# Optimization experiments

Measured on AMD Instinct MI355X. Metric: run time of the kernel, lower is better.

The kernel has to match this reference:

```python
import jax, jax.numpy as jnp
import numpy as np

EPS = 1e-5

def exp_map_zero(v):
    # Poincare ball exp map at origin: tanh(||v||) * v / ||v||
    norm = jnp.clip(jnp.linalg.norm(v, axis=-1, keepdims=True), EPS, None)
    return jnp.tanh(jnp.clip(norm, None, 15.0)) * v / norm

def poincare_pairwise_distance(x, c):
    # x: [N, D] points in the ball, c: [K, D] points in the ball -> [N, K]
    x2 = jnp.sum(x * x, axis=-1)                      # [N]
    c2 = jnp.sum(c * c, axis=-1)                      # [K]
    sqdiff = x2[:, None] + c2[None, :] - 2.0 * (x @ c.T)   # ||x-c||^2, [N, K]
    sqdiff = jnp.clip(sqdiff, 0.0, None)
    denom = jnp.clip((1.0 - x2)[:, None] * (1.0 - c2)[None, :], EPS, None)
    arg = jnp.clip(1.0 + 2.0 * sqdiff / denom, 1.0 + 1e-7, None)
    return jnp.arccosh(arg)

def setup_inputs() -> dict:
    key = jax.random.key(0)
    k1, k2, k3 = jax.random.split(key, 3)
    N, K, D = 200000, 128, 128
    node_repr = jax.random.normal(k1, (N, D), dtype=jnp.float32) * 0.05  # inside unit ball
    mask = jnp.ones((N, 1), dtype=jnp.float32)
    centroid_weight = jax.random.normal(k2, (K, D), dtype=jnp.float32) * 0.05
    return {"node_repr": node_repr, "mask": mask, "centroid_weight": centroid_weight}

def reference(node_repr, mask, centroid_weight):
    # euclidean embed_manifold path: map centroid params onto the ball first
    centroid_repr = exp_map_zero(centroid_weight)                  # [K, D]
    dist = poincare_pairwise_distance(node_repr, centroid_repr)    # [N, K]
    node_centroid_dist = dist[None, :, :] * mask                   # [1, N, K] (mask [N,1] broadcasts)
    graph_centroid_dist = jnp.sum(node_centroid_dist, axis=1) / jnp.sum(mask)  # [1, K]
    return (graph_centroid_dist, node_centroid_dist)
```

## Files before the change

### kernel.cpp

```cpp
#include <hip/hip_runtime.h>
#include <hip/hip_bf16.h>
#include <math.h>

#define EPSF 1e-5f

constexpr int D = 128;
constexpr int K = 128;
constexpr int ROWS_PER_BLOCK = 64;

typedef __bf16 bf16x8 __attribute__((ext_vector_type(8)));
typedef float  f32x4  __attribute__((ext_vector_type(4)));

__global__ __launch_bounds__(64) void prep_kernel(const float* __restrict__ w,
                                                  __bf16* __restrict__ crb,
                                                  float* __restrict__ c2) {
    int k = blockIdx.x;
    int t = threadIdx.x;
    float a = w[k * D + t];
    float b = w[k * D + t + 64];
    float ss = a * a + b * b;
#pragma unroll
    for (int off = 1; off < 64; off <<= 1)
        ss += __shfl_xor(ss, off, 64);
    float nrm   = sqrtf(ss);
    float nclip = fmaxf(nrm, EPSF);
    float targ  = fminf(nclip, 15.0f);
    float th    = tanhf(targ);
    float s     = th / nclip;
    crb[k * D + t]      = (__bf16)(a * s);
    crb[k * D + t + 64] = (__bf16)(b * s);
    if (t == 0) {
        float cn = s * nrm;
        c2[k] = cn * cn;
    }
}

__global__ __launch_bounds__(256) void main_kernel(
        const float* __restrict__ x, const float* __restrict__ mask,
        const __bf16* __restrict__ crb, const float* __restrict__ c2g,
        float* __restrict__ out_node, float* __restrict__ partial,
        float* __restrict__ maskpart, int N) {
    __shared__ float sX2[ROWS_PER_BLOCK];
    __shared__ float sMask[ROWS_PER_BLOCK];
    __shared__ float sC2[K];
    __shared__ float sCol[4][K];

    const int t    = threadIdx.x;
    const int wave = t >> 6;
    const int lane = t & 63;
    const int m    = lane & 15;
    const int q    = lane >> 4;
    const int nbase   = blockIdx.x * ROWS_PER_BLOCK;
    const int rowbase = nbase + wave * 16;

    if (t < ROWS_PER_BLOCK) sMask[t] = mask[nbase + t];
    if (t < K) sC2[t] = c2g[t];

    const float*  xrow = x + (size_t)(rowbase + m) * D + q * 8;
    const __bf16* cb   = crb + (size_t)m * D + q * 8;

    f32x4 acc[8] = {};
    float ssq = 0.f;

#pragma unroll
    for (int s = 0; s < 4; s++) {
        float4 a0 = *(const float4*)(xrow + s * 32);
        float4 a1 = *(const float4*)(xrow + s * 32 + 4);
        ssq += a0.x*a0.x + a0.y*a0.y + a0.z*a0.z + a0.w*a0.w
             + a1.x*a1.x + a1.y*a1.y + a1.z*a1.z + a1.w*a1.w;
        bf16x8 av;
        av[0] = (__bf16)a0.x; av[1] = (__bf16)a0.y;
        av[2] = (__bf16)a0.z; av[3] = (__bf16)a0.w;
        av[4] = (__bf16)a1.x; av[5] = (__bf16)a1.y;
        av[6] = (__bf16)a1.z; av[7] = (__bf16)a1.w;
#pragma unroll
        for (int tk = 0; tk < 8; tk++) {
            bf16x8 bv = *(const bf16x8*)(cb + ((size_t)tk * 16) * D + s * 32);
            acc[tk] = __builtin_amdgcn_mfma_f32_16x16x32_bf16(av, bv, acc[tk], 0, 0, 0);
        }
    }

    ssq += __shfl_xor(ssq, 16, 64);
    ssq += __shfl_xor(ssq, 32, 64);
    if (lane < 16) sX2[wave * 16 + lane] = ssq;
    __syncthreads();

    float x2r[4], pxr[4], mvr[4];
#pragma unroll
    for (int i = 0; i < 4; i++) {
        int rl = wave * 16 + q * 4 + i;
        x2r[i] = sX2[rl];
        pxr[i] = 1.0f - x2r[i];
        mvr[i] = sMask[rl];
    }

    float colsum[8] = {0.f, 0.f, 0.f, 0.f, 0.f, 0.f, 0.f, 0.f};
#pragma unroll
    for (int tk = 0; tk < 8; tk++) {
        int col = tk * 16 + m;
        float c2v = sC2[col];
        float pc  = 1.0f - c2v;
#pragma unroll
        for (int i = 0; i < 4; i++) {
            int n = rowbase + q * 4 + i;
            float dot = acc[tk][i];
            float sq  = fmaxf(x2r[i] + c2v - 2.0f * dot, 0.0f);
            float den = fmaxf(pxr[i] * pc, EPSF);
            float arg = fmaf(2.0f * sq, __builtin_amdgcn_rcpf(den), 1.0f);
            arg = fmaxf(arg, 1.0f + 1e-7f);
            float dist = __logf(arg + __builtin_amdgcn_sqrtf(fmaf(arg, arg, -1.0f)));
            float val = dist * mvr[i];
            out_node[(size_t)n * K + col] = val;
            colsum[tk] += val;
        }
    }

#pragma unroll
    for (int tk = 0; tk < 8; tk++) {
        colsum[tk] += __shfl_xor(colsum[tk], 16, 64);
        colsum[tk] += __shfl_xor(colsum[tk], 32, 64);
    }
    if (lane < 16) {
#pragma unroll
        for (int tk = 0; tk < 8; tk++)
            sCol[wave][tk * 16 + lane] = colsum[tk];
    }
    __syncthreads();
    if (t < K)
        partial[(size_t)blockIdx.x * K + t] =
            sCol[0][t] + sCol[1][t] + sCol[2][t] + sCol[3][t];
    if (t == 0) {
        float msum = 0.f;
#pragma unroll
        for (int r = 0; r < ROWS_PER_BLOCK; r++) msum += sMask[r];
        maskpart[blockIdx.x] = msum;
    }
}

__global__ __launch_bounds__(256) void reduce_kernel(
        const float* __restrict__ partial, const float* __restrict__ maskpart,
        float* __restrict__ out_graph, int NB) {
    int k = blockIdx.x;
    int t = threadIdx.x;
    float s = 0.f, mm = 0.f;
    for (int b = t; b < NB; b += 256) {
        s  += partial[(size_t)b * K + k];
        mm += maskpart[b];
    }
#pragma unroll
    for (int off = 1; off < 64; off <<= 1) {
        s  += __shfl_xor(s, off, 64);
        mm += __shfl_xor(mm, off, 64);
    }
    __shared__ float rs[4], rm[4];
    int w = t >> 6;
    if ((t & 63) == 0) { rs[w] = s; rm[w] = mm; }
    __syncthreads();
    if (t == 0) {
        float st = rs[0] + rs[1] + rs[2] + rs[3];
        float mt = rm[0] + rm[1] + rm[2] + rm[3];
        out_graph[k] = st / mt;
    }
}

extern "C" void kernel_launch(void* const* d_in, const int* in_sizes, int n_in,
                              void* d_out, int out_size, void* d_ws, size_t ws_size,
                              hipStream_t stream) {
    const float* node = (const float*)d_in[0];
    const float* mask = (const float*)d_in[1];
    const float* w    = (const float*)d_in[2];
    float* out = (float*)d_out;

    int N  = in_sizes[0] / D;
    int NB = N / ROWS_PER_BLOCK;

    __bf16* crb     = (__bf16*)d_ws;
    float* c2       = (float*)(crb + K * D);
    float* partial  = c2 + K;
    float* maskpart = partial + (size_t)NB * K;

    float* out_graph = out;
    float* out_node  = out + K;

    prep_kernel<<<K, 64, 0, stream>>>(w, crb, c2);
    main_kernel<<<NB, 256, 0, stream>>>(node, mask, crb, c2, out_node,
                                        partial, maskpart, N);
    reduce_kernel<<<K, 256, 0, stream>>>(partial, maskpart, out_graph, NB);
}
```

Baseline: 231.2 us.

## Stage centroid matrix in padded LDS, prefetch x rows, defer nontemporal output stores

Each block now copies the bf16 centroid matrix into shared memory with a padded pitch, so the MFMA B operands come from LDS without bank conflicts instead of from global/L2. All x loads are issued up front before the staging, and the distance values are held in registers and written at the end with nontemporal stores to keep the streaming output from polluting the cache. This costs about 34 KB of LDS per block, which may lower occupancy, plus extra registers for the buffered outputs.

```diff
diff --git a/kernel.cpp b/kernel.cpp
--- a/kernel.cpp
+++ b/kernel.cpp
@@ -7,6 +7,7 @@
 constexpr int D = 128;
 constexpr int K = 128;
 constexpr int ROWS_PER_BLOCK = 64;
+constexpr int BPITCH = 272;
 
 typedef __bf16 bf16x8 __attribute__((ext_vector_type(8)));
 typedef float  f32x4  __attribute__((ext_vector_type(4)));
@@ -40,6 +41,7 @@
         const __bf16* __restrict__ crb, const float* __restrict__ c2g,
         float* __restrict__ out_node, float* __restrict__ partial,
         float* __restrict__ maskpart, int N) {
+    __shared__ __align__(16) unsigned char sB[K * BPITCH];
     __shared__ float sX2[ROWS_PER_BLOCK];
     __shared__ float sMask[ROWS_PER_BLOCK];
     __shared__ float sC2[K];
@@ -53,37 +55,52 @@
     const int nbase   = blockIdx.x * ROWS_PER_BLOCK;
     const int rowbase = nbase + wave * 16;
 
+    const float* xrow = x + (size_t)(rowbase + m) * D + q * 8;
+    float4 xr[8];
+#pragma unroll
+    for (int s = 0; s < 4; s++) {
+        xr[2 * s]     = *(const float4*)(xrow + s * 32);
+        xr[2 * s + 1] = *(const float4*)(xrow + s * 32 + 4);
+    }
+
+#pragma unroll
+    for (int i = 0; i < 8; i++) {
+        int f4  = t + 256 * i;
+        int row = f4 >> 4;
+        int c4  = f4 & 15;
+        float4 v = ((const float4*)crb)[f4];
+        *(float4*)(sB + row * BPITCH + c4 * 16) = v;
+    }
     if (t < ROWS_PER_BLOCK) sMask[t] = mask[nbase + t];
     if (t < K) sC2[t] = c2g[t];
 
-    const float*  xrow = x + (size_t)(rowbase + m) * D + q * 8;
-    const __bf16* cb   = crb + (size_t)m * D + q * 8;
-
-    f32x4 acc[8] = {};
     float ssq = 0.f;
-
+    bf16x8 av[4];
 #pragma unroll
     for (int s = 0; s < 4; s++) {
-        float4 a0 = *(const float4*)(xrow + s * 32);
-        float4 a1 = *(const float4*)(xrow + s * 32 + 4);
+        float4 a0 = xr[2 * s], a1 = xr[2 * s + 1];
         ssq += a0.x*a0.x + a0.y*a0.y + a0.z*a0.z + a0.w*a0.w
              + a1.x*a1.x + a1.y*a1.y + a1.z*a1.z + a1.w*a1.w;
-        bf16x8 av;
-        av[0] = (__bf16)a0.x; av[1] = (__bf16)a0.y;
-        av[2] = (__bf16)a0.z; av[3] = (__bf16)a0.w;
-        av[4] = (__bf16)a1.x; av[5] = (__bf16)a1.y;
-        av[6] = (__bf16)a1.z; av[7] = (__bf16)a1.w;
-#pragma unroll
-        for (int tk = 0; tk < 8; tk++) {
-            bf16x8 bv = *(const bf16x8*)(cb + ((size_t)tk * 16) * D + s * 32);
-            acc[tk] = __builtin_amdgcn_mfma_f32_16x16x32_bf16(av, bv, acc[tk], 0, 0, 0);
-        }
-    }
-
+        av[s][0] = (__bf16)a0.x; av[s][1] = (__bf16)a0.y;
+        av[s][2] = (__bf16)a0.z; av[s][3] = (__bf16)a0.w;
+        av[s][4] = (__bf16)a1.x; av[s][5] = (__bf16)a1.y;
+        av[s][6] = (__bf16)a1.z; av[s][7] = (__bf16)a1.w;
+    }
     ssq += __shfl_xor(ssq, 16, 64);
     ssq += __shfl_xor(ssq, 32, 64);
     if (lane < 16) sX2[wave * 16 + lane] = ssq;
+
     __syncthreads();
+
+    f32x4 acc[8] = {};
+#pragma unroll
+    for (int s = 0; s < 4; s++) {
+#pragma unroll
+        for (int tk = 0; tk < 8; tk++) {
+            bf16x8 bv = *(const bf16x8*)(sB + (tk * 16 + m) * BPITCH + q * 16 + s * 64);
+            acc[tk] = __builtin_amdgcn_mfma_f32_16x16x32_bf16(av[s], bv, acc[tk], 0, 0, 0);
+        }
+    }
 
     float x2r[4], pxr[4], mvr[4];
 #pragma unroll
@@ -94,15 +111,16 @@
         mvr[i] = sMask[rl];
     }
 
-    float colsum[8] = {0.f, 0.f, 0.f, 0.f, 0.f, 0.f, 0.f, 0.f};
+    float dv[8][4];
+    float colsum[8];
 #pragma unroll
     for (int tk = 0; tk < 8; tk++) {
         int col = tk * 16 + m;
         float c2v = sC2[col];
         float pc  = 1.0f - c2v;
+        colsum[tk] = 0.f;
 #pragma unroll
         for (int i = 0; i < 4; i++) {
-            int n = rowbase + q * 4 + i;
             float dot = acc[tk][i];
             float sq  = fmaxf(x2r[i] + c2v - 2.0f * dot, 0.0f);
             float den = fmaxf(pxr[i] * pc, EPSF);
@@ -110,7 +128,7 @@
             arg = fmaxf(arg, 1.0f + 1e-7f);
             float dist = __logf(arg + __builtin_amdgcn_sqrtf(fmaf(arg, arg, -1.0f)));
             float val = dist * mvr[i];
-            out_node[(size_t)n * K + col] = val;
+            dv[tk][i] = val;
             colsum[tk] += val;
         }
     }
@@ -125,7 +143,9 @@
         for (int tk = 0; tk < 8; tk++)
             sCol[wave][tk * 16 + lane] = colsum[tk];
     }
+
     __syncthreads();
+
     if (t < K)
         partial[(size_t)blockIdx.x * K + t] =
             sCol[0][t] + sCol[1][t] + sCol[2][t] + sCol[3][t];
@@ -134,6 +154,15 @@
 #pragma unroll
         for (int r = 0; r < ROWS_PER_BLOCK; r++) msum += sMask[r];
         maskpart[blockIdx.x] = msum;
+    }
+#pragma unroll
+    for (int tk = 0; tk < 8; tk++) {
+        int col = tk * 16 + m;
+#pragma unroll
+        for (int i = 0; i < 4; i++) {
+            int n = rowbase + q * 4 + i;
+            __builtin_nontemporal_store(dv[tk][i], &out_node[(size_t)n * K + col]);
+        }
     }
 }
 
```

After: 196.5 us. 1.18x faster.

## Make main kernel persistent with centroids staged in padded LDS

Applied to the files above, without the earlier changes.

Replaces the one-block-per-64-rows grid with a fixed grid of 1024 persistent blocks whose waves stride over 16-row tiles. The bf16 centroid matrix is loaded once per block into padded shared memory, and centroid norms and reciprocals are kept in registers. Per-row norms and mask values are passed by wave shuffles instead of shared memory and barriers. The output stores become nontemporal and the denominator clamp is replaced by a product of reciprocals. This cuts repeated global/L2 reads of the centroids and the block launch and reduction overhead, at the cost of dropping the EPS clamp on the denominator and about 35 KB of LDS per block.

```diff
diff --git a/kernel.cpp b/kernel.cpp
--- a/kernel.cpp
+++ b/kernel.cpp
@@ -6,7 +6,8 @@
 
 constexpr int D = 128;
 constexpr int K = 128;
-constexpr int ROWS_PER_BLOCK = 64;
+constexpr int BPITCH = 272;
+constexpr int NBLK = 1024;
 
 typedef __bf16 bf16x8 __attribute__((ext_vector_type(8)));
 typedef float  f32x4  __attribute__((ext_vector_type(4)));
@@ -35,83 +36,99 @@
     }
 }
 
-__global__ __launch_bounds__(256) void main_kernel(
+__global__ __launch_bounds__(256, 4) void main_kernel(
         const float* __restrict__ x, const float* __restrict__ mask,
         const __bf16* __restrict__ crb, const float* __restrict__ c2g,
         float* __restrict__ out_node, float* __restrict__ partial,
         float* __restrict__ maskpart, int N) {
-    __shared__ float sX2[ROWS_PER_BLOCK];
-    __shared__ float sMask[ROWS_PER_BLOCK];
-    __shared__ float sC2[K];
+    __shared__ __align__(16) unsigned char sB[K * BPITCH];
     __shared__ float sCol[4][K];
+    __shared__ float sMaskW[4];
 
     const int t    = threadIdx.x;
     const int wave = t >> 6;
     const int lane = t & 63;
     const int m    = lane & 15;
     const int q    = lane >> 4;
-    const int nbase   = blockIdx.x * ROWS_PER_BLOCK;
-    const int rowbase = nbase + wave * 16;
-
-    if (t < ROWS_PER_BLOCK) sMask[t] = mask[nbase + t];
-    if (t < K) sC2[t] = c2g[t];
-
-    const float*  xrow = x + (size_t)(rowbase + m) * D + q * 8;
-    const __bf16* cb   = crb + (size_t)m * D + q * 8;
-
-    f32x4 acc[8] = {};
-    float ssq = 0.f;
-
-#pragma unroll
-    for (int s = 0; s < 4; s++) {
-        float4 a0 = *(const float4*)(xrow + s * 32);
-        float4 a1 = *(const float4*)(xrow + s * 32 + 4);
-        ssq += a0.x*a0.x + a0.y*a0.y + a0.z*a0.z + a0.w*a0.w
-             + a1.x*a1.x + a1.y*a1.y + a1.z*a1.z + a1.w*a1.w;
-        bf16x8 av;
-        av[0] = (__bf16)a0.x; av[1] = (__bf16)a0.y;
-        av[2] = (__bf16)a0.z; av[3] = (__bf16)a0.w;
-        av[4] = (__bf16)a1.x; av[5] = (__bf16)a1.y;
-        av[6] = (__bf16)a1.z; av[7] = (__bf16)a1.w;
+
+#pragma unroll
+    for (int i = 0; i < 8; i++) {
+        int f4  = t + 256 * i;
+        int row = f4 >> 4;
+        int c4  = f4 & 15;
+        float4 v = ((const float4*)crb)[f4];
+        *(float4*)(sB + row * BPITCH + c4 * 16) = v;
+    }
+
+    float c2r[8], rpc[8];
+#pragma unroll
+    for (int tk = 0; tk < 8; tk++) {
+        c2r[tk] = c2g[tk * 16 + m];
+        rpc[tk] = __builtin_amdgcn_rcpf(1.0f - c2r[tk]);
+    }
+
+    __syncthreads();
+
+    const int ntiles = N >> 4;
+    const int stride = NBLK * 4;
+    float colsum[8] = {0.f, 0.f, 0.f, 0.f, 0.f, 0.f, 0.f, 0.f};
+    float masksum = 0.f;
+
+    for (int tile = blockIdx.x * 4 + wave; tile < ntiles; tile += stride) {
+        const int rowbase = tile * 16;
+        const float* xrow = x + (size_t)(rowbase + m) * D + q * 8;
+        float mv = mask[rowbase + m];
+
+        f32x4 acc[8] = {};
+        float ssq = 0.f;
+#pragma unroll
+        for (int s = 0; s < 4; s++) {
+            float4 a0 = *(const float4*)(xrow + s * 32);
+            float4 a1 = *(const float4*)(xrow + s * 32 + 4);
+            ssq += a0.x*a0.x + a0.y*a0.y + a0.z*a0.z + a0.w*a0.w
+                 + a1.x*a1.x + a1.y*a1.y + a1.z*a1.z + a1.w*a1.w;
+            bf16x8 av;
+            av[0] = (__bf16)a0.x; av[1] = (__bf16)a0.y;
+            av[2] = (__bf16)a0.z; av[3] = (__bf16)a0.w;
+            av[4] = (__bf16)a1.x; av[5] = (__bf16)a1.y;
+            av[6] = (__bf16)a1.z; av[7] = (__bf16)a1.w;
+#pragma unroll
+            for (int tk = 0; tk < 8; tk++) {
+                bf16x8 bv = *(const bf16x8*)(sB + (tk * 16 + m) * BPITCH + q * 16 + s * 64);
+                acc[tk] = __builtin_amdgcn_mfma_f32_16x16x32_bf16(av, bv, acc[tk], 0, 0, 0);
+            }
+        }
+
+        ssq += __shfl_xor(ssq, 16, 64);
+        ssq += __shfl_xor(ssq, 32, 64);
+        float rpxm = __builtin_amdgcn_rcpf(1.0f - ssq);
+
+        float x2r[4], rpx[4], mvr[4];
+#pragma unroll
+        for (int i = 0; i < 4; i++) {
+            int src = q * 4 + i;
+            x2r[i] = __shfl(ssq,  src, 64);
+            rpx[i] = __shfl(rpxm, src, 64);
+            mvr[i] = __shfl(mv,   src, 64);
+        }
+        masksum += mv;
+
 #pragma unroll
         for (int tk = 0; tk < 8; tk++) {
-            bf16x8 bv = *(const bf16x8*)(cb + ((size_t)tk * 16) * D + s * 32);
-            acc[tk] = __builtin_amdgcn_mfma_f32_16x16x32_bf16(av, bv, acc[tk], 0, 0, 0);
-        }
-    }
-
-    ssq += __shfl_xor(ssq, 16, 64);
-    ssq += __shfl_xor(ssq, 32, 64);
-    if (lane < 16) sX2[wave * 16 + lane] = ssq;
-    __syncthreads();
-
-    float x2r[4], pxr[4], mvr[4];
-#pragma unroll
-    for (int i = 0; i < 4; i++) {
-        int rl = wave * 16 + q * 4 + i;
-        x2r[i] = sX2[rl];
-        pxr[i] = 1.0f - x2r[i];
-        mvr[i] = sMask[rl];
-    }
-
-    float colsum[8] = {0.f, 0.f, 0.f, 0.f, 0.f, 0.f, 0.f, 0.f};
-#pragma unroll
-    for (int tk = 0; tk < 8; tk++) {
-        int col = tk * 16 + m;
-        float c2v = sC2[col];
-        float pc  = 1.0f - c2v;
-#pragma unroll
-        for (int i = 0; i < 4; i++) {
-            int n = rowbase + q * 4 + i;
-            float dot = acc[tk][i];
-            float sq  = fmaxf(x2r[i] + c2v - 2.0f * dot, 0.0f);
-            float den = fmaxf(pxr[i] * pc, EPSF);
-            float arg = fmaf(2.0f * sq, __builtin_amdgcn_rcpf(den), 1.0f);
-            arg = fmaxf(arg, 1.0f + 1e-7f);
-            float dist = __logf(arg + __builtin_amdgcn_sqrtf(fmaf(arg, arg, -1.0f)));
-            float val = dist * mvr[i];
-            out_node[(size_t)n * K + col] = val;
-            colsum[tk] += val;
+            int col = tk * 16 + m;
+            float c2v = c2r[tk];
+#pragma unroll
+            for (int i = 0; i < 4; i++) {
+                float dot = acc[tk][i];
+                float sq  = fmaxf(fmaf(-2.0f, dot, x2r[i] + c2v), 0.0f);
+                float arg = fmaf(2.0f * sq, rpx[i] * rpc[tk], 1.0f);
+                arg = fmaxf(arg, 1.0f + 1e-7f);
+                float dist = __logf(arg + __builtin_amdgcn_sqrtf(fmaf(arg, arg, -1.0f)));
+                float val = dist * mvr[i];
+                colsum[tk] += val;
+                int n = rowbase + q * 4 + i;
+                __builtin_nontemporal_store(val, &out_node[(size_t)n * K + col]);
+            }
         }
     }
 
@@ -125,16 +142,16 @@
         for (int tk = 0; tk < 8; tk++)
             sCol[wave][tk * 16 + lane] = colsum[tk];
     }
+#pragma unroll
+    for (int off = 1; off < 64; off <<= 1)
+        masksum += __shfl_xor(masksum, off, 64);
+    if (lane == 0) sMaskW[wave] = masksum * 0.25f;
     __syncthreads();
     if (t < K)
         partial[(size_t)blockIdx.x * K + t] =
             sCol[0][t] + sCol[1][t] + sCol[2][t] + sCol[3][t];
-    if (t == 0) {
-        float msum = 0.f;
-#pragma unroll
-        for (int r = 0; r < ROWS_PER_BLOCK; r++) msum += sMask[r];
-        maskpart[blockIdx.x] = msum;
-    }
+    if (t == 0)
+        maskpart[blockIdx.x] = sMaskW[0] + sMaskW[1] + sMaskW[2] + sMaskW[3];
 }
 
 __global__ __launch_bounds__(256) void reduce_kernel(
@@ -171,19 +188,18 @@
     const float* w    = (const float*)d_in[2];
     float* out = (float*)d_out;
 
-    int N  = in_sizes[0] / D;
-    int NB = N / ROWS_PER_BLOCK;
+    int N = in_sizes[0] / D;
 
     __bf16* crb     = (__bf16*)d_ws;
     float* c2       = (float*)(crb + K * D);
     float* partial  = c2 + K;
-    float* maskpart = partial + (size_t)NB * K;
+    float* maskpart = partial + (size_t)NBLK * K;
 
     float* out_graph = out;
     float* out_node  = out + K;
 
     prep_kernel<<<K, 64, 0, stream>>>(w, crb, c2);
-    main_kernel<<<NB, 256, 0, stream>>>(node, mask, crb, c2, out_node,
-                                        partial, maskpart, N);
-    reduce_kernel<<<K, 256, 0, stream>>>(partial, maskpart, out_graph, NB);
-}
+    main_kernel<<<NBLK, 256, 0, stream>>>(node, mask, crb, c2, out_node,
+                                          partial, maskpart, N);
+    reduce_kernel<<<K, 256, 0, stream>>>(partial, maskpart, out_graph, NBLK);
+}
```

Result: slower. 270.5 us (+17.0%).
